# Kernel optimization log

Measured on AMD Instinct MI355X. Metric: run time of the kernel, lower is better.

## Reference

```python
import jax, jax.numpy as jnp
import numpy as np

FEAT_DIM = 1024
NUM_HEAD = 8


def setup_inputs() -> dict:
    key = jax.random.key(0)
    ks = jax.random.split(key, 8)
    D = FEAT_DIM
    s = D ** -0.5
    return {
        "motion": jax.random.normal(ks[0], (8, 1024, D), dtype=jnp.float32),
        "scene_feats": jax.random.normal(ks[1], (8, 2048, D), dtype=jnp.float32),
        # nn.Linear weights stored as [in, out] (already transposed for x @ W)
        "Wq": jax.random.normal(ks[2], (D, D), dtype=jnp.float32) * s,
        "bq": jax.random.normal(ks[3], (D,), dtype=jnp.float32) * s,
        "Wkv": jax.random.normal(ks[4], (D, 2 * D), dtype=jnp.float32) * s,
        "bkv": jax.random.normal(ks[5], (2 * D,), dtype=jnp.float32) * s,
        "Wout": jax.random.normal(ks[6], (D, D), dtype=jnp.float32) * s,
        "bout": jax.random.normal(ks[7], (D,), dtype=jnp.float32) * s,
    }


def reference(motion, scene_feats, Wq, bq, Wkv, bkv, Wout, bout):
    bs, L, D = motion.shape
    N = scene_feats.shape[1]
    H = NUM_HEAD
    Dh = D // H

    # q scaled by full feat_dim**-0.5 (as in source, not head_dim)
    q = (motion @ Wq + bq) * (D ** -0.5)
    kv = scene_feats @ Wkv + bkv
    k, v = kv[..., :D], kv[..., D:]

    # Faithful to source: q is viewed as (bs, H, L, Dh) with NO transpose,
    # while k, v use view(bs, N, H, Dh) followed by transpose(1, 2).
    q = q.reshape(bs, H, L, Dh)                      # [bs,H,L,Dh] (layout quirk)
    k = k.reshape(bs, N, H, Dh).transpose(0, 2, 1, 3)  # [bs,H,N,Dh]
    v = v.reshape(bs, N, H, Dh).transpose(0, 2, 1, 3)  # [bs,H,N,Dh]

    att = jnp.einsum("bhld,bhnd->bhln", q, k)        # [bs,H,L,N]
    att = jax.nn.softmax(att, axis=-1)
    out = jnp.einsum("bhln,bhnd->bhld", att, v)      # [bs,H,L,Dh]
    out = out.reshape(bs, L, D)                      # contiguous view, matches torch .view
    return out @ Wout + bout
```

## Files before the change

### kernel.cpp

```cpp
#include <hip/hip_runtime.h>

typedef __attribute__((ext_vector_type(8))) short bf16x8;
typedef __attribute__((ext_vector_type(4))) float f32x4;
typedef __attribute__((ext_vector_type(4))) float f32x4v;

#define MFMA16(a,b,c) __builtin_amdgcn_mfma_f32_16x16x32_bf16((a),(b),(c),0,0,0)

__device__ __forceinline__ short f2bf(float f){
  unsigned u = __builtin_bit_cast(unsigned, f);
  u += 0x7fffu + ((u >> 16) & 1u);
  return (short)(u >> 16);
}

__device__ __forceinline__ void gload16(const void* g, void* l){
  __builtin_amdgcn_global_load_lds((const __attribute__((address_space(1))) unsigned*)g,
                                   (__attribute__((address_space(3))) unsigned*)l,
                                   16, 0, 0);
}

__global__ __launch_bounds__(256) void k_f2bf(const float* __restrict__ in,
                                              short* __restrict__ out, int n8){
  int i = blockIdx.x * 256 + threadIdx.x;
  if (i >= n8) return;
  f32x4v a = ((const f32x4v*)in)[i*2];
  f32x4v b = ((const f32x4v*)in)[i*2+1];
  bf16x8 o;
  o[0]=f2bf(a[0]); o[1]=f2bf(a[1]); o[2]=f2bf(a[2]); o[3]=f2bf(a[3]);
  o[4]=f2bf(b[0]); o[5]=f2bf(b[1]); o[6]=f2bf(b[2]); o[7]=f2bf(b[3]);
  ((bf16x8*)out)[i] = o;
}

__global__ __launch_bounds__(256) void k_prep_wT(const float* __restrict__ W,
                                                 short* __restrict__ Wt, int K, int N){
  int i = blockIdx.x * 256 + threadIdx.x;
  int total = (K >> 3) * N;
  if (i >= total) return;
  int n  = i % N;
  int k0 = (i / N) << 3;
  bf16x8 o;
#pragma unroll
  for (int j = 0; j < 8; ++j) o[j] = f2bf(W[(size_t)(k0 + j) * N + n]);
  *(bf16x8*)&Wt[(size_t)n * K + k0] = o;
}

template<int MODE>
__global__ __launch_bounds__(256, 4) void k_gemm(
    const short* __restrict__ A, const short* __restrict__ Bt,
    const float* __restrict__ bias, float scale,
    void* __restrict__ out0, void* __restrict__ out1,
    int M, int N, int K)
{
  __shared__ __align__(16) short Alds[4][128 * 32];
  __shared__ __align__(16) short Blds[4][128 * 32];
  const int tid = threadIdx.x;
  const int l = tid & 63, w = tid >> 6;
  const int wr = w >> 1, wc = w & 1;
  const int lr = l & 15, lg = l >> 4;

  const int nx = gridDim.x;
  const int nwg = nx * gridDim.y;
  int flat = blockIdx.y * nx + blockIdx.x;
  int u = (flat & 7) * (nwg >> 3) + (flat >> 3);
  const int m0 = (u / nx) * 128, n0 = (u % nx) * 128;

  const int srow = l >> 2;
  const int scol = 8 * ((l & 3) ^ ((l >> 3) & 3));
  const int acol = 8 * (lg ^ ((lr >> 1) & 3));

  f32x4 acc[4][4];
#pragma unroll
  for (int a = 0; a < 4; ++a)
#pragma unroll
    for (int b = 0; b < 4; ++b) acc[a][b] = (f32x4)(0.0f);

  const int nk = K >> 5;
  auto stage = [&](int kt, int slot){
    int k0 = kt << 5;
#pragma unroll
    for (int i = 0; i < 4; ++i){
      int c = w * 4 + i;
      if (c < 8){
        int m = c * 16 + srow;
        gload16(A + (size_t)(m0 + m) * K + k0 + scol, &Alds[slot][c * 512]);
      } else {
        int n = (c - 8) * 16 + srow;
        gload16(Bt + (size_t)(n0 + n) * K + k0 + scol, &Blds[slot][(c - 8) * 512]);
      }
    }
  };

  stage(0, 0);
  stage(1, 1);
  stage(2, 2);
  int rd = 0;
  for (int kt = 0; kt < nk; ++kt){
    asm volatile("s_waitcnt vmcnt(8)" ::: "memory");
    __builtin_amdgcn_s_barrier();
    int tt = (kt + 3 < nk) ? kt + 3 : nk - 1;
    int tgt = (rd + 3) & 3;
    stage(tt, tgt);

    bf16x8 af[4], bfv[4];
#pragma unroll
    for (int mi = 0; mi < 4; ++mi){
      int row = wr * 64 + mi * 16 + lr;
      af[mi] = *(const bf16x8*)&Alds[rd][row * 32 + acol];
    }
#pragma unroll
    for (int ni = 0; ni < 4; ++ni){
      int row = wc * 64 + ni * 16 + lr;
      bfv[ni] = *(const bf16x8*)&Blds[rd][row * 32 + acol];
    }
#pragma unroll
    for (int mi = 0; mi < 4; ++mi)
#pragma unroll
      for (int ni = 0; ni < 4; ++ni)
        acc[mi][ni] = MFMA16(af[mi], bfv[ni], acc[mi][ni]);

    rd = (rd + 1) & 3;
  }
  asm volatile("s_waitcnt vmcnt(0)" ::: "memory");

#pragma unroll
  for (int mi = 0; mi < 4; ++mi)
#pragma unroll
    for (int ni = 0; ni < 4; ++ni){
      int col = n0 + wc * 64 + ni * 16 + lr;
      float bv = bias[col];
#pragma unroll
      for (int r = 0; r < 4; ++r){
        int row = m0 + wr * 64 + mi * 16 + lg * 4 + r;
        float v = acc[mi][ni][r] + bv;
        if (MODE == 0){
          v *= scale;
          int b = row >> 10, lp = row & 1023;
          int h = lp >> 7;
          int lq = ((lp & 127) << 3) | (col >> 7);
          int dh = col & 127;
          ((short*)out0)[(((size_t)(b * 8 + h)) * 1024 + lq) * 128 + dh] = f2bf(v);
        } else if (MODE == 1){
          int b = row >> 11, nn = row & 2047;
          if (col < 1024){
            int h = col >> 7, dh = col & 127;
            ((short*)out0)[(((size_t)(b * 8 + h)) * 2048 + nn) * 128 + dh] = f2bf(v);
          } else {
            int c2 = col - 1024, h = c2 >> 7, dh = c2 & 127;
            ((short*)out1)[(((size_t)(b * 8 + h)) * 128 + dh) * 2048 + nn] = f2bf(v);
          }
        } else {
          ((float*)out0)[(size_t)row * N + col] = v;
        }
      }
    }
}

__global__ __launch_bounds__(512, 2) void k_attn(
    const short* __restrict__ Q, const short* __restrict__ K,
    const short* __restrict__ Vt, short* __restrict__ O)
{
  __shared__ __align__(16) short Klds[2][64 * 128];
  __shared__ __align__(16) short Vlds[2][128 * 64];
  __shared__ __align__(16) short Plds[8][32 * 64];
  const int tid = threadIdx.x;
  const int l = tid & 63, w = tid >> 6;
  const int lr = l & 15, lg = l >> 4;

  int flat = blockIdx.y * 4 + blockIdx.x;
  int xcd = flat & 7, idx = flat >> 3;
  int bh = xcd * 8 + (idx >> 2);
  int q0 = (idx & 3) * 256;

  const short* Qb = Q  + (size_t)bh * 1024 * 128;
  const short* Kb = K  + (size_t)bh * 2048 * 128;
  const short* Vb = Vt + (size_t)bh * 128 * 2048;

  bf16x8 qf[2][4];
#pragma unroll
  for (int mi = 0; mi < 2; ++mi)
#pragma unroll
    for (int kc = 0; kc < 4; ++kc)
      qf[mi][kc] = *(const bf16x8*)&Qb[(size_t)(q0 + w * 32 + mi * 16 + lr) * 128 + kc * 32 + lg * 8];

  f32x4 acc[8][2];
#pragma unroll
  for (int d = 0; d < 8; ++d){ acc[d][0] = (f32x4)(0.0f); acc[d][1] = (f32x4)(0.0f); }
  float mrun[2][4], lsum[2][4];
#pragma unroll
  for (int mi = 0; mi < 2; ++mi)
#pragma unroll
    for (int r = 0; r < 4; ++r){ mrun[mi][r] = -3e38f; lsum[mi][r] = 0.f; }

  auto stageK = [&](int t, int buf){
    int kv0 = t * 64;
#pragma unroll
    for (int i = 0; i < 2; ++i){
      int c = w * 2 + i;
      int row = 4 * c + (l >> 4);
      int col = ((l & 15) * 8) ^ ((row & 7) * 8);
      gload16(Kb + (size_t)(kv0 + row) * 128 + col, &Klds[buf][c * 512]);
    }
  };
  auto stageV = [&](int t, int buf){
    int kv0 = t * 64;
#pragma unroll
    for (int i = 0; i < 2; ++i){
      int c = w * 2 + i;
      int dh = 8 * c + (l >> 3);
      int col = ((l & 7) * 8) ^ (((l >> 3) & 7) * 8);
      gload16(Vb + (size_t)dh * 2048 + kv0 + col, &Vlds[buf][c * 512]);
    }
  };

  stageK(0, 0); stageV(0, 0);
  __syncthreads();
  int cur = 0;
  const int swz = (lr & 7) * 8;

  for (int t = 0; t < 32; ++t){
    if (t + 1 < 32){ stageK(t + 1, cur ^ 1); stageV(t + 1, cur ^ 1); }
    const short* Kl = &Klds[cur][0];
    const short* Vl = &Vlds[cur][0];
    short* Pw = &Plds[w][0];

    f32x4 s[2][4];
    __builtin_amdgcn_s_setprio(1);
#pragma unroll
    for (int nt = 0; nt < 4; ++nt){
      f32x4 s0 = (f32x4)(0.0f), s1 = (f32x4)(0.0f);
#pragma unroll
      for (int kc = 0; kc < 4; ++kc){
        bf16x8 kf = *(const bf16x8*)&Kl[(nt * 16 + lr) * 128 + ((kc * 32 + lg * 8) ^ swz)];
        s0 = MFMA16(qf[0][kc], kf, s0);
        s1 = MFMA16(qf[1][kc], kf, s1);
      }
      s[0][nt] = s0; s[1][nt] = s1;
    }
    __builtin_amdgcn_s_setprio(0);

    float pmax[2][4];
    int ok = 1;
#pragma unroll
    for (int mi = 0; mi < 2; ++mi)
#pragma unroll
      for (int r = 0; r < 4; ++r){
        float v = fmaxf(fmaxf(s[mi][0][r], s[mi][1][r]), fmaxf(s[mi][2][r], s[mi][3][r]));
        pmax[mi][r] = v;
        ok &= (v <= mrun[mi][r] + 8.0f) ? 1 : 0;
      }
    if (!__all(ok)){
#pragma unroll
      for (int mi = 0; mi < 2; ++mi)
#pragma unroll
        for (int r = 0; r < 4; ++r){
          float v = pmax[mi][r];
          v = fmaxf(v, __shfl_xor(v, 1, 16));
          v = fmaxf(v, __shfl_xor(v, 2, 16));
          v = fmaxf(v, __shfl_xor(v, 4, 16));
          v = fmaxf(v, __shfl_xor(v, 8, 16));
          float mnew = fmaxf(mrun[mi][r], v);
          float sc = exp2f(mrun[mi][r] - mnew);
          mrun[mi][r] = mnew;
          lsum[mi][r] *= sc;
#pragma unroll
          for (int d = 0; d < 8; ++d) acc[d][mi][r] *= sc;
        }
    }

#pragma unroll
    for (int mi = 0; mi < 2; ++mi)
#pragma unroll
      for (int r = 0; r < 4; ++r){
        int row = mi * 16 + lg * 4 + r;
        int rsw = (row & 7) * 8;
        float ls = 0.f;
#pragma unroll
        for (int nt = 0; nt < 4; ++nt){
          float p = exp2f(s[mi][nt][r] - mrun[mi][r]);
          ls += p;
          Pw[row * 64 + ((nt * 16 + lr) ^ rsw)] = f2bf(p);
        }
        lsum[mi][r] += ls;
      }

    bf16x8 pa[2][2];
#pragma unroll
    for (int mi = 0; mi < 2; ++mi)
#pragma unroll
      for (int kc = 0; kc < 2; ++kc)
        pa[mi][kc] = *(const bf16x8*)&Pw[(mi * 16 + lr) * 64 + ((kc * 32 + lg * 8) ^ swz)];
    __builtin_amdgcn_s_setprio(1);
#pragma unroll
    for (int d = 0; d < 8; ++d)
#pragma unroll
      for (int kc = 0; kc < 2; ++kc){
        bf16x8 vf = *(const bf16x8*)&Vl[(d * 16 + lr) * 64 + ((kc * 32 + lg * 8) ^ swz)];
        acc[d][0] = MFMA16(pa[0][kc], vf, acc[d][0]);
        acc[d][1] = MFMA16(pa[1][kc], vf, acc[d][1]);
      }
    __builtin_amdgcn_s_setprio(0);

    __syncthreads();
    cur ^= 1;
  }

  const int b = bh >> 3, h = bh & 7;
#pragma unroll
  for (int mi = 0; mi < 2; ++mi)
#pragma unroll
    for (int r = 0; r < 4; ++r){
      float ls = lsum[mi][r];
      ls += __shfl_xor(ls, 1, 16);
      ls += __shfl_xor(ls, 2, 16);
      ls += __shfl_xor(ls, 4, 16);
      ls += __shfl_xor(ls, 8, 16);
      float inv = 1.0f / ls;
      int grow = q0 + w * 32 + mi * 16 + lg * 4 + r;
      size_t base = ((size_t)b * 1024 + (size_t)h * 128 + (grow >> 3)) * 1024
                  + (size_t)(grow & 7) * 128;
#pragma unroll
      for (int d = 0; d < 8; ++d)
        O[base + d * 16 + lr] = f2bf(acc[d][mi][r] * inv);
    }
}

extern "C" void kernel_launch(void* const* d_in, const int* in_sizes, int n_in,
                              void* d_out, int out_size, void* d_ws, size_t ws_size,
                              hipStream_t stream){
  const float* motion = (const float*)d_in[0];
  const float* scene  = (const float*)d_in[1];
  const float* Wq     = (const float*)d_in[2];
  const float* bq     = (const float*)d_in[3];
  const float* Wkv    = (const float*)d_in[4];
  const float* bkv    = (const float*)d_in[5];
  const float* Wout   = (const float*)d_in[6];
  const float* bout   = (const float*)d_in[7];
  float* out = (float*)d_out;

  char* ws = (char*)d_ws;
  const size_t MB = 1024 * 1024;
  short* WqT   = (short*)(ws + 0);
  short* WkvT  = (short*)(ws + 2  * MB);
  short* WoutT = (short*)(ws + 6  * MB);
  short* mA    = (short*)(ws + 8  * MB);
  short* sA    = (short*)(ws + 24 * MB);
  short* Qb    = (short*)(ws + 56 * MB);
  short* Kb    = (short*)(ws + 72 * MB);
  short* Vtb   = (short*)(ws + 104* MB);
  short* attnO = mA;

  const float qscale = 0.03125f * 1.44269504088896341f;

  k_prep_wT<<<dim3(512),  256, 0, stream>>>(Wq,   WqT,   1024, 1024);
  k_prep_wT<<<dim3(1024), 256, 0, stream>>>(Wkv,  WkvT,  1024, 2048);
  k_prep_wT<<<dim3(512),  256, 0, stream>>>(Wout, WoutT, 1024, 1024);
  k_f2bf<<<dim3(4096), 256, 0, stream>>>(motion, mA, 1024 * 1024);
  k_f2bf<<<dim3(8192), 256, 0, stream>>>(scene,  sA, 2 * 1024 * 1024);

  k_gemm<0><<<dim3(8, 64),   256, 0, stream>>>(mA, WqT,  bq,  qscale, Qb, nullptr, 8192, 1024, 1024);
  k_gemm<1><<<dim3(16, 128), 256, 0, stream>>>(sA, WkvT, bkv, 1.0f,   Kb, Vtb,    16384, 2048, 1024);
  k_attn<<<dim3(4, 64), 512, 0, stream>>>(Qb, Kb, Vtb, attnO);
  k_gemm<2><<<dim3(8, 64), 256, 0, stream>>>(attnO, WoutT, bout, 1.0f, out, nullptr, 8192, 1024, 1024);
}
```

Before: 313.8 us.

## Add dedicated 256x256-tile KV projection GEMM and shrink GEMM pipeline to three stages

Replaces the KV projection GEMM, the largest of the three projections, with a dedicated 512-thread kernel using 256x256 output tiles. Each wave computes 128x64, which raises arithmetic intensity per LDS load, and MFMA issue priority is raised with setprio. The generic GEMM drops from a four-slot to a three-slot LDS ring with two tiles in flight, which cuts its LDS use and may allow more blocks per CU. The trade-off is less latency hiding in the generic GEMM and higher register pressure in the new kernel from its 32 accumulators.

```diff
diff --git a/kernel.cpp b/kernel.cpp
--- a/kernel.cpp
+++ b/kernel.cpp
@@ -50,8 +50,8 @@
     void* __restrict__ out0, void* __restrict__ out1,
     int M, int N, int K)
 {
-  __shared__ __align__(16) short Alds[4][128 * 32];
-  __shared__ __align__(16) short Blds[4][128 * 32];
+  __shared__ __align__(16) short Alds[3][128 * 32];
+  __shared__ __align__(16) short Blds[3][128 * 32];
   const int tid = threadIdx.x;
   const int l = tid & 63, w = tid >> 6;
   const int wr = w >> 1, wc = w & 1;
@@ -91,13 +91,13 @@
 
   stage(0, 0);
   stage(1, 1);
-  stage(2, 2);
   int rd = 0;
   for (int kt = 0; kt < nk; ++kt){
-    asm volatile("s_waitcnt vmcnt(8)" ::: "memory");
+    asm volatile("s_waitcnt vmcnt(4)" ::: "memory");
     __builtin_amdgcn_s_barrier();
-    int tt = (kt + 3 < nk) ? kt + 3 : nk - 1;
-    int tgt = (rd + 3) & 3;
+    __builtin_amdgcn_sched_barrier(0);
+    int tt = (kt + 2 < nk) ? kt + 2 : nk - 1;
+    int tgt = rd + 2; if (tgt >= 3) tgt -= 3;
     stage(tt, tgt);
 
     bf16x8 af[4], bfv[4];
@@ -117,7 +117,7 @@
       for (int ni = 0; ni < 4; ++ni)
         acc[mi][ni] = MFMA16(af[mi], bfv[ni], acc[mi][ni]);
 
-    rd = (rd + 1) & 3;
+    if (++rd == 3) rd = 0;
   }
   asm volatile("s_waitcnt vmcnt(0)" ::: "memory");
 
@@ -138,17 +138,105 @@
           int lq = ((lp & 127) << 3) | (col >> 7);
           int dh = col & 127;
           ((short*)out0)[(((size_t)(b * 8 + h)) * 1024 + lq) * 128 + dh] = f2bf(v);
-        } else if (MODE == 1){
-          int b = row >> 11, nn = row & 2047;
-          if (col < 1024){
-            int h = col >> 7, dh = col & 127;
-            ((short*)out0)[(((size_t)(b * 8 + h)) * 2048 + nn) * 128 + dh] = f2bf(v);
-          } else {
-            int c2 = col - 1024, h = c2 >> 7, dh = c2 & 127;
-            ((short*)out1)[(((size_t)(b * 8 + h)) * 128 + dh) * 2048 + nn] = f2bf(v);
-          }
         } else {
           ((float*)out0)[(size_t)row * N + col] = v;
+        }
+      }
+    }
+}
+
+__global__ __launch_bounds__(512, 2) void k_gemmKV(
+    const short* __restrict__ A, const short* __restrict__ Bt,
+    const float* __restrict__ bias,
+    short* __restrict__ out0, short* __restrict__ out1)
+{
+  __shared__ __align__(16) short As[3][256 * 32];
+  __shared__ __align__(16) short Bs[3][256 * 32];
+  const int tid = threadIdx.x;
+  const int l = tid & 63, w = tid >> 6;
+  const int lr = l & 15, lg = l >> 4;
+  const int wm = w >> 2, wn = w & 3;
+
+  int flat = blockIdx.y * 8 + blockIdx.x;
+  int u = (flat & 7) * 64 + (flat >> 3);
+  const int m0 = (u >> 3) * 256, n0 = (u & 7) * 256;
+
+  const int srow = l >> 2;
+  const int scol = 8 * ((l & 3) ^ ((l >> 3) & 3));
+  const int acol = 8 * (lg ^ ((lr >> 1) & 3));
+
+  f32x4 acc[8][4];
+#pragma unroll
+  for (int a = 0; a < 8; ++a)
+#pragma unroll
+    for (int b = 0; b < 4; ++b) acc[a][b] = (f32x4)(0.0f);
+
+  auto stage = [&](int kt, int slot){
+    int k0 = kt << 5;
+#pragma unroll
+    for (int i = 0; i < 4; ++i){
+      int c = w * 4 + i;
+      if (c < 16){
+        int m = c * 16 + srow;
+        gload16(A + (size_t)(m0 + m) * 1024 + k0 + scol, &As[slot][c * 512]);
+      } else {
+        int n = (c - 16) * 16 + srow;
+        gload16(Bt + (size_t)(n0 + n) * 1024 + k0 + scol, &Bs[slot][(c - 16) * 512]);
+      }
+    }
+  };
+
+  stage(0, 0);
+  stage(1, 1);
+  int rd = 0;
+  for (int kt = 0; kt < 32; ++kt){
+    asm volatile("s_waitcnt vmcnt(4)" ::: "memory");
+    __builtin_amdgcn_s_barrier();
+    __builtin_amdgcn_sched_barrier(0);
+    int tt = (kt + 2 < 32) ? kt + 2 : 31;
+    int tgt = rd + 2; if (tgt >= 3) tgt -= 3;
+    stage(tt, tgt);
+
+    bf16x8 af[8], bfv[4];
+#pragma unroll
+    for (int mi = 0; mi < 8; ++mi){
+      int row = wm * 128 + mi * 16 + lr;
+      af[mi] = *(const bf16x8*)&As[rd][row * 32 + acol];
+    }
+#pragma unroll
+    for (int ni = 0; ni < 4; ++ni){
+      int row = wn * 64 + ni * 16 + lr;
+      bfv[ni] = *(const bf16x8*)&Bs[rd][row * 32 + acol];
+    }
+    __builtin_amdgcn_s_setprio(1);
+#pragma unroll
+    for (int mi = 0; mi < 8; ++mi)
+#pragma unroll
+      for (int ni = 0; ni < 4; ++ni)
+        acc[mi][ni] = MFMA16(af[mi], bfv[ni], acc[mi][ni]);
+    __builtin_amdgcn_s_setprio(0);
+
+    if (++rd == 3) rd = 0;
+  }
+  asm volatile("s_waitcnt vmcnt(0)" ::: "memory");
+
+#pragma unroll
+  for (int mi = 0; mi < 8; ++mi)
+#pragma unroll
+    for (int ni = 0; ni < 4; ++ni){
+      int col = n0 + wn * 64 + ni * 16 + lr;
+      float bv = bias[col];
+#pragma unroll
+      for (int r = 0; r < 4; ++r){
+        int row = m0 + wm * 128 + mi * 16 + lg * 4 + r;
+        float v = acc[mi][ni][r] + bv;
+        int b = row >> 11, nn = row & 2047;
+        if (col < 1024){
+          int h = col >> 7, dh = col & 127;
+          out0[(((size_t)(b * 8 + h)) * 2048 + nn) * 128 + dh] = f2bf(v);
+        } else {
+          int c2 = col - 1024, h = c2 >> 7, dh = c2 & 127;
+          out1[(((size_t)(b * 8 + h)) * 128 + dh) * 2048 + nn] = f2bf(v);
         }
       }
     }
@@ -356,8 +444,8 @@
   k_f2bf<<<dim3(4096), 256, 0, stream>>>(motion, mA, 1024 * 1024);
   k_f2bf<<<dim3(8192), 256, 0, stream>>>(scene,  sA, 2 * 1024 * 1024);
 
-  k_gemm<0><<<dim3(8, 64),   256, 0, stream>>>(mA, WqT,  bq,  qscale, Qb, nullptr, 8192, 1024, 1024);
-  k_gemm<1><<<dim3(16, 128), 256, 0, stream>>>(sA, WkvT, bkv, 1.0f,   Kb, Vtb,    16384, 2048, 1024);
+  k_gemm<0><<<dim3(8, 64), 256, 0, stream>>>(mA, WqT, bq, qscale, Qb, nullptr, 8192, 1024, 1024);
+  k_gemmKV<<<dim3(8, 64), 512, 0, stream>>>(sA, WkvT, bkv, Kb, Vtb);
   k_attn<<<dim3(4, 64), 512, 0, stream>>>(Qb, Kb, Vtb, attnO);
   k_gemm<2><<<dim3(8, 64), 256, 0, stream>>>(attnO, WoutT, bout, 1.0f, out, nullptr, 8192, 1024, 1024);
 }
```

After: 303.6 us. 3.2% less time.
